# Kernel optimization log

Hardware: AMD Instinct MI355X
Metric: run time of the kernel (lower is better)

The kernel has to match this reference:

```python
import jax, jax.numpy as jnp
import numpy as np

B=16; NW=17; NR=116; WS=10; E=128; LNUM=5; NEXP=4; TOPK=2; DS=16
LAM=0.01; EPS=1e-5
ED=NW*WS      # 170 expert dim
SEQ=NR*WS     # 1160

def softshrink(x, l):
    return jnp.sign(x) * jnp.maximum(jnp.abs(x) - l, 0.0)

def layernorm(x, g, b):
    m = x.mean(-1, keepdims=True)
    v = ((x - m) ** 2).mean(-1, keepdims=True)
    return (x - m) / jnp.sqrt(v + EPS) * g + b

def sscan(x, A, WB, WC, Wdt, D):
    # Mamba-style selective scan. x: [L, d], A/WB/WC: [d, n] / [d, n_state]
    dt = jax.nn.softplus(x @ Wdt)          # [L, d]
    Bt = x @ WB                            # [L, n]
    Ct = x @ WC                            # [L, n]
    def step(h, inp):
        xt, dtt, bt, ct = inp
        dA = jnp.exp(dtt[:, None] * A)     # [d, n]
        h = dA * h + (dtt * xt)[:, None] * bt[None, :]
        y = (h * ct[None, :]).sum(-1) + D * xt
        return h, y
    h0 = jnp.zeros((x.shape[1], A.shape[1]), x.dtype)
    _, y = jax.lax.scan(step, h0, (x, dt, Bt, Ct))
    return y                               # [L, d]

def setup_inputs() -> dict:
    key = jax.random.key(0)
    ks = jax.random.split(key, 32)
    r = lambda i, sh, s=1.0: jax.random.normal(ks[i], sh, dtype=jnp.float32) * s
    return {
        'win_seq': r(0, (B, NW, NR, WS)),
        'win_pcc': r(1, (B, NR, NR, NW)),
        'global_adjs': jax.random.uniform(ks[2], (B, NR, NR), dtype=jnp.float32) / NR,
        'patch_adjs': jax.random.uniform(ks[3], (B, NW * NR, NW * NR), dtype=jnp.float32) / (NW * NR),
        'embeddings': r(4, (E,)),
        'fgc_w': r(5, (NW, LNUM, 2, E, E), 0.02),
        'fgc_b': r(6, (NW, LNUM, 2, E), 0.02),
        'w_c': r(7, (NW, E), 0.01),
        'ln_g': jnp.ones((SEQ,), jnp.float32), 'ln_b': jnp.zeros((SEQ,), jnp.float32),
        'A1': -(jax.random.uniform(ks[8], (NR, DS), dtype=jnp.float32) + 0.5),
        'WB1': r(9, (NR, DS), 0.1), 'WC1': r(10, (NR, DS), 0.1),
        'Wdt1': r(11, (NR, NR), 0.1), 'D1': jnp.ones((NR,), jnp.float32),
        'Wout1': r(12, (NW, NR, SEQ), 0.02),
        'A2': -(jax.random.uniform(ks[13], (SEQ, DS), dtype=jnp.float32) + 0.5),
        'WB2': r(14, (SEQ, DS), 0.03), 'WC2': r(15, (SEQ, DS), 0.03),
        'Wdt2': r(16, (SEQ, SEQ), 0.01), 'D2': jnp.ones((SEQ,), jnp.float32),
        'Wout2': r(17, (SEQ, SEQ), 0.02),
        'W_gate': r(18, (2 * ED, ED), 0.05), 'b_gate': jnp.zeros((ED,), jnp.float32),
        'rln_g': jnp.ones((ED,), jnp.float32), 'rln_b': jnp.zeros((ED,), jnp.float32),
        'Wr': r(19, (ED, NEXP), 0.05), 'br': jnp.zeros((NEXP,), jnp.float32),
        'We': r(20, (NEXP, ED, ED), 0.06),
        'W1': r(21, (NR * ED, 512), 0.01), 'b1': jnp.zeros((512,), jnp.float32),
        'W2': r(22, (512, 256), 0.05), 'b2': jnp.zeros((256,), jnp.float32),
        'W3': r(23, (256, 128), 0.06), 'b3': jnp.zeros((128,), jnp.float32),
        'W4': r(24, (128, 2), 0.09), 'b4': jnp.zeros((2,), jnp.float32),
    }

def reference(win_seq, win_pcc, global_adjs, patch_adjs, embeddings, fgc_w, fgc_b, w_c,
              ln_g, ln_b, A1, WB1, WC1, Wdt1, D1, Wout1, A2, WB2, WC2, Wdt2, D2, Wout2,
              W_gate, b_gate, rln_g, rln_b, Wr, br, We, W1, b1, W2, b2, W3, b3, W4, b4):
    Bsz = win_seq.shape[0]
    # tokenEmb: [B,NW,SEQ] -> [B,NW,SEQ,E]
    x = win_seq.reshape(Bsz, NW, SEQ)[..., None] * embeddings
    xf = jnp.fft.rfft(x, axis=2, norm='ortho')
    # fourierGC: 5 complex dense layers per window with relu + softshrink
    for l in range(LNUM):
        wr = fgc_w[:, l, 0]; wi = fgc_w[:, l, 1]
        br_ = fgc_b[:, l, 0]; bi_ = fgc_b[:, l, 1]
        o_r = jax.nn.relu(jnp.einsum('bwfi,wij->bwfj', xf.real, wr)
                          - jnp.einsum('bwfi,wij->bwfj', xf.imag, wi) + br_[None, :, None, :])
        o_i = jax.nn.relu(jnp.einsum('bwfi,wij->bwfj', xf.imag, wr)
                          + jnp.einsum('bwfi,wij->bwfj', xf.real, wi) + bi_[None, :, None, :])
        xf = jax.lax.complex(softshrink(o_r, LAM), softshrink(o_i, LAM))
    x = jnp.fft.irfft(xf, n=SEQ, axis=2, norm='ortho')      # [B,NW,SEQ,E]
    x = x.reshape(Bsz, NW, NR, WS, E)
    # channel-softmax pooling over embed dim (per-window w_c)
    wc = jax.nn.softmax(w_c, axis=-1)                        # [NW,E]
    freq_feat = jnp.einsum('bwnte,we->bwnt', x, wc).reshape(Bsz, NW, SEQ)

    # DGSM1: selective scan over mean-PCC node features
    x1 = win_pcc.mean(-1)                                    # [B,NR,NR]
    y1 = jax.vmap(lambda a: sscan(a, A1, WB1, WC1, Wdt1, D1))(x1)
    pooled = y1.mean(axis=1)                                 # [B,NR]
    out1 = jnp.einsum('bd,wdk->bwk', pooled, Wout1)          # [B,NW,SEQ]

    # DGSM2: graph propagation (global adjacency on roi dim) + scan over windows
    x2 = freq_feat.reshape(Bsz, NW, NR, WS)
    x2 = jnp.einsum('bnm,bwmf->bwnf', global_adjs, x2).reshape(Bsz, NW, SEQ)
    y2 = jax.vmap(lambda a: sscan(a, A2, WB2, WC2, Wdt2, D2))(x2)
    out2 = y2 @ Wout2                                        # [B,NW,SEQ]

    time_feat = layernorm(out1, ln_g, ln_b).reshape(Bsz, NW, NR, WS)
    freq2 = layernorm(out2, ln_g, ln_b).reshape(Bsz, NW, NR, WS)
    cat = jnp.concatenate([freq2, time_feat], -1).transpose(0, 2, 1, 3).reshape(Bsz, NR, 2 * ED)
    gate = jax.nn.sigmoid(cat @ W_gate + b_gate)             # [B,NR,ED]
    fp = freq2.transpose(0, 2, 1, 3).reshape(Bsz, NR, ED)
    tp = time_feat.transpose(0, 2, 1, 3).reshape(Bsz, NR, ED)
    fusion = gate * fp + (1.0 - gate) * tp                   # [B,NR,ED]

    # top-k MoE with GCN experts on global adjacency
    logits = layernorm(fusion, rln_g, rln_b) @ Wr + br       # [B,NR,NEXP]
    vals, idx = jax.lax.top_k(logits, TOPK)
    w = jax.nn.softmax(vals, axis=-1)
    gates = (jax.nn.one_hot(idx, NEXP, dtype=fusion.dtype) * w[..., None]).sum(-2)
    support = jnp.einsum('bnf,efg->beng', fusion, We)
    eout = jax.nn.relu(jnp.einsum('bnm,bemg->beng', global_adjs, support))
    moe = jnp.einsum('beng,bne->bng', eout, gates)           # [B,NR,ED]

    # classifier head; BatchNorm in eval mode with fresh running stats = x/sqrt(1+eps)
    bn_scale = 1.0 / (1.0 + EPS) ** 0.5
    h = jax.nn.relu((moe.reshape(Bsz, -1) @ W1 + b1) * bn_scale)
    h = jax.nn.relu((h @ W2 + b2) * bn_scale)
    h = jax.nn.relu((h @ W3 + b3) * bn_scale)
    return h @ W4 + b4                                       # [B,2]
```

## Files before the change

### kernel.cpp

```cpp
#include <hip/hip_runtime.h>
#include <math.h>

#define BSZ 16
#define NWW 17
#define NRR 116
#define WSS 10
#define EMB 128
#define LAYN 5
#define DST 16
#define SEQL 1160
#define FRQ 581
#define EDD 170
#define LAMW 0.01f
#define EPSW 1e-5f
#define NBW (BSZ*NWW)

#define SXF 1024.0f
#define SWF 4096.0f
#define INVS 2.384185791015625e-07f

typedef _Float16 half8 __attribute__((ext_vector_type(8)));
typedef float float4v __attribute__((ext_vector_type(4)));

__device__ __forceinline__ float softplus_f(float x){
    return fmaxf(x, 0.f) + log1pf(expf(-fabsf(x)));
}
__device__ __forceinline__ float sigmoid_f(float x){
    return 1.f / (1.f + expf(-x));
}

__global__ void k_tables(float* tc, float* ts){
    int k = blockIdx.x*256 + threadIdx.x;
    if (k < SEQL){
        double th = (6.283185307179586476925286766559 * (double)k) / (double)SEQL;
        tc[k] = (float)cos(th);
        ts[k] = (float)sin(th);
    }
}
__global__ void k_mk_tmaj(const float* tc, const float* ts, float* Ct, float* St){
    int id = blockIdx.x*256 + threadIdx.x;
    if (id >= SEQL*FRQ) return;
    int f = id % FRQ, t = id / FRQ;
    int idx = (f*t) % SEQL;
    Ct[id] = tc[idx]; St[id] = ts[idx];
}
__global__ void k_mk_fmaj(const float* tc, const float* ts, float* Cf, float* Sf){
    int id = blockIdx.x*256 + threadIdx.x;
    if (id >= SEQL*FRQ) return;
    int t = id % SEQL, f = id / SEQL;
    int idx = (f*t) % SEQL;
    Cf[id] = tc[idx]; Sf[id] = ts[idx];
}

__global__ void k_wcsm(const float* w_c, float* wcs){
    int w = blockIdx.x; int j = threadIdx.x;
    __shared__ float red[EMB];
    float v = w_c[w*EMB + j];
    red[j] = v; __syncthreads();
    for (int s = 64; s > 0; s >>= 1){ if (j < s) red[j] = fmaxf(red[j], red[j+s]); __syncthreads(); }
    float m = red[0]; __syncthreads();
    float e = expf(v - m);
    red[j] = e; __syncthreads();
    for (int s = 64; s > 0; s >>= 1){ if (j < s) red[j] += red[j+s]; __syncthreads(); }
    wcs[w*EMB + j] = e / red[0];
}

__global__ void k_ew(const float* emb, const float* fgc_w, float* ewr, float* ewi){
    int id = blockIdx.x*256 + threadIdx.x;
    if (id >= NWW*EMB) return;
    int w = id / EMB, j = id % EMB;
    const float* wr = fgc_w + ((size_t)(w*LAYN + 0)*2 + 0)*EMB*EMB;
    const float* wi = wr + (size_t)EMB*EMB;
    float ar = 0.f, ai = 0.f;
    for (int i = 0; i < EMB; i++){
        float e = emb[i];
        ar += e * wr[i*EMB + j];
        ai += e * wi[i*EMB + j];
    }
    ewr[id] = ar; ewi[id] = ai;
}

#define DFT_TCH 290
__global__ void k_dft(const float* ws, const float* Ct, const float* St,
                      float* pre, float* pim){
    __shared__ float X[4][DFT_TCH];
    int f = blockIdx.x*256 + threadIdx.x;
    int bw0 = blockIdx.y*4;
    int t0 = blockIdx.z*DFT_TCH;
    for (int e = threadIdx.x; e < 4*DFT_TCH; e += 256){
        int g = e / DFT_TCH, t = e % DFT_TCH;
        X[g][t] = ws[(size_t)(bw0+g)*SEQL + t0 + t];
    }
    __syncthreads();
    if (f >= FRQ) return;
    float sr[4] = {0,0,0,0}, si[4] = {0,0,0,0};
    #pragma unroll 2
    for (int tt = 0; tt < DFT_TCH; tt++){
        int t = t0 + tt;
        float ct_ = Ct[(size_t)t*FRQ + f];
        float st_ = St[(size_t)t*FRQ + f];
        #pragma unroll
        for (int g = 0; g < 4; g++){
            sr[g] += X[g][tt]*ct_;
            si[g] += X[g][tt]*st_;
        }
    }
    size_t base = (size_t)blockIdx.z*NBW;
    #pragma unroll
    for (int g = 0; g < 4; g++){
        pre[(base + bw0+g)*FRQ + f] = sr[g];
        pim[(base + bw0+g)*FRQ + f] = si[g];
    }
}

__global__ void k_wprep(const float* fgc_w, _Float16* Wpk){
// ... 19 lines not shown
        half8 hv, lv;
        #pragma unroll
        for (int jj = 0; jj < 8; jj++){
            int k = kc*32 + q*8 + jj;
            float v = T[k][n];
            _Float16 h = (_Float16)v;
            hv[jj] = h; lv[jj] = (_Float16)(v - (float)h);
        }
        *(half8*)&hi[d0] = hv;
        *(half8*)&lo[d0] = lv;
    }
}

#define AIDX(row, jc) (((row)<<7) + ((((jc) ^ ((row)&15))) << 3))
#define OLD 132
__launch_bounds__(256, 3)
__global__ void k_fgc_fused(const float* pre, const float* pim,
                            const float* ewr, const float* ewi,
                            const float* fgc_b, const float* wcs,
                            const _Float16* Wpk,
                            float* zre, float* zim){
    __shared__ __align__(16) _Float16 AhR[32*128];
    __shared__ __align__(16) _Float16 AlR[32*128];
    __shared__ __align__(16) _Float16 AhI[32*128];
    __shared__ __align__(16) _Float16 AlI[32*128];
    __shared__ __align__(16) float OUTR[16*OLD];
    __shared__ __align__(16) float OUTI[16*OLD];
    int tid = threadIdx.x;
    int by = blockIdx.y; int w = by >> 4; int b = by & 15;
    int bw = b*NWW + w;
    int f0 = blockIdx.x * 32;
    int lane = tid & 63, wv = tid >> 6;
    int c = lane & 15, q = lane >> 4;

    {
        int f = tid >> 3;
        int j0 = (tid & 7) << 4;
        int fg = f0 + f;
        float re = 0.f, im = 0.f;
        if (fg < FRQ){
            size_t o = (size_t)bw*FRQ + fg;
            const size_t PS = (size_t)NBW*FRQ;
            float r  = pre[o] + pre[PS+o] + pre[2*PS+o] + pre[3*PS+o];
            float i_ = pim[o] + pim[PS+o] + pim[2*PS+o] + pim[3*PS+o];
            const float sc = 0.02936128f;
            re = r * sc;
            im = -i_ * sc;
        }
        const float* br = fgc_b + (size_t)(w*LAYN + 0)*2*EMB;
        const float* bi = br + EMB;
        #pragma unroll
        for (int g = 0; g < 2; g++){
            half8 hR, lR, hI, lI;
            #pragma unroll
            for (int u = 0; u < 8; u++){
                int jj = j0 + g*8 + u;
                float er = ewr[w*EMB + jj], ei = ewi[w*EMB + jj];
                float xr = fmaxf(re*er - im*ei + br[jj] - LAMW, 0.f) * SXF;
                float xi = fmaxf(im*er + re*ei + bi[jj] - LAMW, 0.f) * SXF;
                _Float16 h1 = (_Float16)xr; hR[u] = h1; lR[u] = (_Float16)(xr - (float)h1);
                _Float16 h2 = (_Float16)xi; hI[u] = h2; lI[u] = (_Float16)(xi - (float)h2);
            }
            int jc = (tid & 7)*2 + g;
            int ao = AIDX(f, jc);
            *(half8*)&AhR[ao] = hR;
            *(half8*)&AlR[ao] = lR;
            *(half8*)&AhI[ao] = hI;
            *(half8*)&AlI[ao] = lI;
        }
    }
    __syncthreads();

    for (int l = 1; l <= 4; l++){
        const _Float16* Wb = Wpk + (size_t)(w*4 + (l-1))*65536;
        float4v Prr[2][2], Pii[2][2], Pri[2][2], Pir[2][2];
        #pragma unroll
        for (int rt = 0; rt < 2; rt++)
            #pragma unroll
            for (int ct = 0; ct < 2; ct++){
                #pragma unroll
                for (int u = 0; u < 4; u++){
                    Prr[rt][ct][u] = 0.f; Pii[rt][ct][u] = 0.f;
                    Pri[rt][ct][u] = 0.f; Pir[rt][ct][u] = 0.f;
                }
            }
        for (int kc = 0; kc < 4; kc++){
            half8 ahR[2], alR[2], ahI[2], alI[2];
            #pragma unroll
            for (int rt = 0; rt < 2; rt++){
                int ao = AIDX(rt*16 + c, kc*4 + q);
                ahR[rt] = *(const half8*)&AhR[ao];
                alR[rt] = *(const half8*)&AlR[ao];
                ahI[rt] = *(const half8*)&AhI[ao];
                alI[rt] = *(const half8*)&AlI[ao];
            }
            #pragma unroll
            for (int ct = 0; ct < 2; ct++){
                int off = ((wv*2 + ct)*2048) + kc*512 + lane*8;
                half8 whR = *(const half8*)&Wb[off];
                half8 wlR = *(const half8*)&Wb[16384 + off];
                half8 whI = *(const half8*)&Wb[32768 + off];
                half8 wlI = *(const half8*)&Wb[49152 + off];
                #pragma unroll
                for (int rt = 0; rt < 2; rt++){
                    Prr[rt][ct] = __builtin_amdgcn_mfma_f32_16x16x32_f16(ahR[rt], whR, Prr[rt][ct], 0,0,0);
                    Prr[rt][ct] = __builtin_amdgcn_mfma_f32_16x16x32_f16(ahR[rt], wlR, Prr[rt][ct], 0,0,0);
                    Prr[rt][ct] = __builtin_amdgcn_mfma_f32_16x16x32_f16(alR[rt], whR, Prr[rt][ct], 0,0,0);
                    Pii[rt][ct] = __builtin_amdgcn_mfma_f32_16x16x32_f16(ahI[rt], whI, Pii[rt][ct], 0,0,0);
                    Pii[rt][ct] = __builtin_amdgcn_mfma_f32_16x16x32_f16(ahI[rt], wlI, Pii[rt][ct], 0,0,0);
                    Pii[rt][ct] = __builtin_amdgcn_mfma_f32_16x16x32_f16(alI[rt], whI, Pii[rt][ct], 0,0,0);
                    Pri[rt][ct] = __builtin_amdgcn_mfma_f32_16x16x32_f16(ahR[rt], whI, Pri[rt][ct], 0,0,0);
                    Pri[rt][ct] = __builtin_amdgcn_mfma_f32_16x16x32_f16(ahR[rt], wlI, Pri[rt][ct], 0,0,0);
                    Pri[rt][ct] = __builtin_amdgcn_mfma_f32_16x16x32_f16(alR[rt], whI, Pri[rt][ct], 0,0,0);
                    Pir[rt][ct] = __builtin_amdgcn_mfma_f32_16x16x32_f16(ahI[rt], whR, Pir[rt][ct], 0,0,0);
                    Pir[rt][ct] = __builtin_amdgcn_mfma_f32_16x16x32_f16(ahI[rt], wlR, Pir[rt][ct], 0,0,0);
                    Pir[rt][ct] = __builtin_amdgcn_mfma_f32_16x16x32_f16(alI[rt], whR, Pir[rt][ct], 0,0,0);
                }
            }
        }
        __syncthreads();
        const float* bR = fgc_b + (size_t)(w*LAYN + l)*2*EMB;
        const float* bI = bR + EMB;
        #pragma unroll
        for (int chunk = 0; chunk < 2; chunk++){
            #pragma unroll
            for (int ct = 0; ct < 2; ct++){
                int n = wv*32 + ct*16 + c;
                float biasR = bR[n] - LAMW, biasI = bI[n] - LAMW;
                #pragma unroll
                for (int r = 0; r < 4; r++){
                    int row = q*4 + r;
                    float vR = (Prr[chunk][ct][r] - Pii[chunk][ct][r])*INVS + biasR;
                    float vI = (Pir[chunk][ct][r] + Pri[chunk][ct][r])*INVS + biasI;
                    OUTR[row*OLD + n] = fmaxf(vR, 0.f);
                    OUTI[row*OLD + n] = fmaxf(vI, 0.f);
                }
            }
            __syncthreads();
            if (l < 4){
                int fch = tid >> 4;
                int j0r = (tid & 15) << 3;
                float4v ra = *(const float4v*)&OUTR[fch*OLD + j0r];
                float4v rb = *(const float4v*)&OUTR[fch*OLD + j0r + 4];
                float4v ia = *(const float4v*)&OUTI[fch*OLD + j0r];
                float4v ib = *(const float4v*)&OUTI[fch*OLD + j0r + 4];
                half8 hR, lR, hI, lI;
                #pragma unroll
                for (int u = 0; u < 4; u++){
                    float xr = ra[u] * SXF;
                    float xi = ia[u] * SXF;
                    _Float16 h1 = (_Float16)xr; hR[u] = h1; lR[u] = (_Float16)(xr - (float)h1);
                    _Float16 h2 = (_Float16)xi; hI[u] = h2; lI[u] = (_Float16)(xi - (float)h2);
                }
                #pragma unroll
                for (int u = 0; u < 4; u++){
                    float xr = rb[u] * SXF;
                    float xi = ib[u] * SXF;
                    _Float16 h1 = (_Float16)xr; hR[4+u] = h1; lR[4+u] = (_Float16)(xr - (float)h1);
                    _Float16 h2 = (_Float16)xi; hI[4+u] = h2; lI[4+u] = (_Float16)(xi - (float)h2);
                }
                int ao = AIDX(chunk*16 + fch, (tid & 15));
                *(half8*)&AhR[ao] = hR;
                *(half8*)&AlR[ao] = lR;
                *(half8*)&AhI[ao] = hI;
                *(half8*)&AlI[ao] = lI;
            } else {
                int fch = tid >> 4;
                int j0r = (tid & 15) << 3;
                float4v ra = *(const float4v*)&OUTR[fch*OLD + j0r];
                float4v rb = *(const float4v*)&OUTR[fch*OLD + j0r + 4];
                float4v ia = *(const float4v*)&OUTI[fch*OLD + j0r];
                float4v ib = *(const float4v*)&OUTI[fch*OLD + j0r + 4];
                float sR = 0.f, sI = 0.f;
                #pragma unroll
                for (int u = 0; u < 4; u++){
                    float cwa = wcs[w*EMB + j0r + u];
                    float cwb = wcs[w*EMB + j0r + 4 + u];
                    sR += ra[u]*cwa + rb[u]*cwb;
                    sI += ia[u]*cwa + ib[u]*cwb;
                }
                #pragma unroll
                for (int o = 8; o > 0; o >>= 1){
                    sR += __shfl_down(sR, o, 64);
                    sI += __shfl_down(sI, o, 64);
                }
                int fg = f0 + chunk*16 + fch;
                if ((tid & 15) == 0 && fg < FRQ){
                    zre[(size_t)bw*FRQ + fg] = sR;
                    zim[(size_t)bw*FRQ + fg] = sI;
                }
            }
            __syncthreads();
        }
    }
}

#define IR_FCH 145
__global__ void k_irfft(const float* zre, const float* zim, const float* Cf, const float* Sf,
                        float* part){
    __shared__ float ZR[4][IR_FCH+1];
    __shared__ float ZI[4][IR_FCH+1];
    int t = blockIdx.x*256 + threadIdx.x;
    int bw0 = blockIdx.y*4;
    int f0 = 1 + blockIdx.z*IR_FCH;
    int fn = min(f0 + IR_FCH, FRQ-1) - f0;
    for (int e = threadIdx.x; e < 4*fn; e += 256){
        int g = e / fn, f = e % fn;
        ZR[g][f] = zre[(size_t)(bw0+g)*FRQ + f0 + f];
        ZI[g][f] = zim[(size_t)(bw0+g)*FRQ + f0 + f];
    }
    __syncthreads();
    if (t >= SEQL) return;
    float acc[4] = {0,0,0,0};
    #pragma unroll 2
    for (int ff_ = 0; ff_ < fn; ff_++){
        int f = f0 + ff_;
        float cf = Cf[(size_t)f*SEQL + t];
        float sf = Sf[(size_t)f*SEQL + t];
        #pragma unroll
        for (int g = 0; g < 4; g++)
            acc[g] += ZR[g][ff_]*cf - ZI[g][ff_]*sf;
    }
    size_t base = (size_t)blockIdx.z*NBW;
    #pragma unroll
    for (int g = 0; g < 4; g++)
        part[(base + bw0+g)*SEQL + t] = acc[g];
}
__global__ void k_irfftc(const float* part, const float* zre, float* ff){
    int id = blockIdx.x*256 + threadIdx.x;
    if (id >= NBW*SEQL) return;
    int t = id % SEQL; int bw = id / SEQL;
    const size_t NS = (size_t)NBW*SEQL;
    float s = part[id] + part[NS + id] + part[2*NS + id] + part[3*NS + id];
// ... 39 lines not shown
    float a = A1[c*DST + s];
    float h = 0.f, csum = 0.f, xsum = 0.f;
    for (int t = 0; t < NRR; t++){
        size_t o = (size_t)(b*NRR + t)*NRR + c;
        float dtv = dt1[o], xv = x1[o];
        size_t ro = (size_t)(b*NRR + t)*DST + s;
        h = expf(dtv*a)*h + dtv*xv*BT1[ro];
        csum += h*CT1[ro];
        xsum += xv;
    }
    #pragma unroll
    for (int o = 8; o > 0; o >>= 1) csum += __shfl_xor(csum, o, 16);
    if (s == 0) pooled[bc] = (csum + D1[c]*xsum) * (1.f/NRR);
}
__global__ void k_out1(const float* pooled, const float* Wout1, float* out1){
    int id = blockIdx.x*256 + threadIdx.x;
    if (id >= NBW*SEQL) return;
    int k = id % SEQL; int bw = id / SEQL; int w = bw % NWW; int b = bw / NWW;
    float s = 0.f;
    for (int d = 0; d < NRR; d++) s += pooled[b*NRR + d] * Wout1[((size_t)w*NRR + d)*SEQL + k];
    out1[id] = s;
}

__global__ void k_ln(const float* in, const float* g, const float* bta, float* out){
    __shared__ float row[SEQL];
    __shared__ float red[256];
    int r = blockIdx.x; int tid = threadIdx.x;
    const float* x = in + (size_t)r*SEQL;
    float s = 0.f;
    for (int i = tid; i < SEQL; i += 256){ float v = x[i]; row[i] = v; s += v; }
    red[tid] = s; __syncthreads();
    for (int st = 128; st > 0; st >>= 1){ if (tid < st) red[tid] += red[tid+st]; __syncthreads(); }
    float m = red[0] * (1.f/SEQL); __syncthreads();
    float vs = 0.f;
    for (int i = tid; i < SEQL; i += 256){ float d = row[i] - m; vs += d*d; }
    red[tid] = vs; __syncthreads();
// ... 26 lines not shown
}

__global__ void k_x2(const float* ga, const float* ff, float* x2){
    int id = blockIdx.x*256 + threadIdx.x;
    if (id >= NBW*SEQL) return;
    int within = id % SEQL; int q = within % WSS; int n = within / WSS;
    int bw = id / SEQL; int w = bw % NWW; int b = bw / NWW;
    const float* gr = ga + ((size_t)b*NRR + n)*NRR;
    const float* fr = ff + (size_t)(b*NWW + w)*SEQL + q;
    float s = 0.f;
    for (int m = 0; m < NRR; m++) s += gr[m] * fr[m*WSS];
    x2[id] = s;
}
#define DT_MCH 290
__global__ void k_dt2(const float* x2, const float* Wdt2, float* part){
    __shared__ float X[4][DT_MCH];
    int c = blockIdx.x*256 + threadIdx.x;
    int bt0 = blockIdx.y*4;
    int m0 = blockIdx.z*DT_MCH;
    for (int e = threadIdx.x; e < 4*DT_MCH; e += 256){
        int g = e / DT_MCH, m = e % DT_MCH;
        X[g][m] = x2[(size_t)(bt0+g)*SEQL + m0 + m];
    }
    __syncthreads();
    if (c >= SEQL) return;
    float a[4] = {0,0,0,0};
    #pragma unroll 2
    for (int mm = 0; mm < DT_MCH; mm++){
        float wv_ = Wdt2[(size_t)(m0+mm)*SEQL + c];
        #pragma unroll
        for (int g = 0; g < 4; g++) a[g] += X[g][mm]*wv_;
    }
    size_t base = (size_t)blockIdx.z*NBW;
    #pragma unroll
    for (int g = 0; g < 4; g++)
        part[(base + bt0+g)*SEQL + c] = a[g];
}
__global__ void k_btct2(const float* x2, const float* WB2, const float* WC2,
                        float* BT2, float* CT2){
    __shared__ float SB[256], SC[256];
    int bt = blockIdx.x;
    int tid = threadIdx.x;
    int s = tid & 15, mc = tid >> 4;
    int m0 = mc*73, m1 = min(m0 + 73, SEQL);
    const float* xr = x2 + (size_t)bt*SEQL;
    float sb = 0.f, sc = 0.f;
    for (int m = m0; m < m1; m++){
        float v = xr[m];
        sb += v*WB2[m*DST + s];
        sc += v*WC2[m*DST + s];
// ... 23 lines not shown
        float dtv = softplus_f(dtp[o] + dtp[NS+o] + dtp[2*NS+o] + dtp[3*NS+o]);
        float xv = x2[o];
        float dx = dtv * xv;
        const float* bt = BT2 + (size_t)(b*NWW + t)*DST;
        const float* ct = CT2 + (size_t)(b*NWW + t)*DST;
        float y = dv * xv;
        #pragma unroll
        for (int s = 0; s < DST; s++){
            h[s] = expf(dtv*a[s])*h[s] + dx*bt[s];
            y += h[s]*ct[s];
        }
        y2[o] = y;
    }
}
__global__ void k_out2(const float* y2, const float* Wout2, float* part){
    __shared__ float Y[4][DT_MCH];
    int k = blockIdx.x*256 + threadIdx.x;
    int bw0 = blockIdx.y*4;
    int m0 = blockIdx.z*DT_MCH;
    for (int e = threadIdx.x; e < 4*DT_MCH; e += 256){
        int g = e / DT_MCH, m = e % DT_MCH;
        Y[g][m] = y2[(size_t)(bw0+g)*SEQL + m0 + m];
    }
    __syncthreads();
    if (k >= SEQL) return;
    float a[4] = {0,0,0,0};
    #pragma unroll 2
    for (int mm = 0; mm < DT_MCH; mm++){
        float wv_ = Wout2[(size_t)(m0+mm)*SEQL + k];
        #pragma unroll
        for (int g = 0; g < 4; g++) a[g] += Y[g][mm]*wv_;
    }
    size_t base = (size_t)blockIdx.z*NBW;
    #pragma unroll
    for (int g = 0; g < 4; g++)
        part[(base + bw0+g)*SEQL + k] = a[g];
}

__global__ void k_gatefusion(const float* fr2, const float* tf, const float* W_gate,
                             const float* b_gate, float* fusion){
    int id = blockIdx.x*256 + threadIdx.x;
    if (id >= BSZ*NRR*EDD) return;
    int j = id % EDD; int n = (id / EDD) % NRR; int b = id / (EDD*NRR);
    float acc = b_gate[j];
    for (int w = 0; w < NWW; w++){
        const float* f2 = fr2 + (size_t)(b*NWW + w)*SEQL + n*WSS;
        const float* tp = tf  + (size_t)(b*NWW + w)*SEQL + n*WSS;
        const float* wg = W_gate + (size_t)(w*2*WSS)*EDD + j;
        #pragma unroll
        for (int q = 0; q < WSS; q++) acc += f2[q]*wg[q*EDD];
// ... 71 lines not shown
    eout[id] = fmaxf(s, 0.f);
}
__global__ void k_moe(const float* eout, const float* gatesE, float* moe){
    int id = blockIdx.x*256 + threadIdx.x;
    if (id >= BSZ*NRR*EDD) return;
    int g = id % EDD; int n = (id / EDD) % NRR; int b = id / (EDD*NRR);
    const float* gt = gatesE + ((size_t)b*NRR + n)*4;
    float s = 0.f;
    #pragma unroll
    for (int e = 0; e < 4; e++)
        s += eout[((size_t)(b*4 + e)*NRR + n)*EDD + g] * gt[e];
    moe[id] = s;
}

#define MLPK (NRR*EDD)
#define KSPLIT 80
#define KCH 247
__global__ void k_mlp1p(const float* moe, const float* W1, float* part1){
    __shared__ float M[16*KCH];
    int kc = blockIdx.x;
    int j = blockIdx.y*256 + threadIdx.x;
    int i0 = kc*KCH; int len = MLPK - i0; if (len > KCH) len = KCH;
    for (int e = threadIdx.x; e < 16*len; e += 256){
        int b = e / len, i = e % len;
        M[b*KCH + i] = moe[(size_t)b*MLPK + i0 + i];
    }
    __syncthreads();
    float acc[16];
    #pragma unroll
    for (int b = 0; b < 16; b++) acc[b] = 0.f;
    for (int i = 0; i < len; i++){
        float wv_ = W1[(size_t)(i0+i)*512 + j];
// ... 76 lines not shown
    const float* We      = (const float*)d_in[28];
    const float* W1      = (const float*)d_in[29];
    const float* b1      = (const float*)d_in[30];
    const float* W2      = (const float*)d_in[31];
    const float* b2      = (const float*)d_in[32];
    const float* W3      = (const float*)d_in[33];
    const float* b3      = (const float*)d_in[34];
    const float* W4      = (const float*)d_in[35];
    const float* b4      = (const float*)d_in[36];
    float* out = (float*)d_out;
    float* ws  = (float*)d_ws;

    size_t off = 0;
    auto alloc = [&](size_t n){ size_t o = off; off += (n + 63) & ~(size_t)63; return o; };
    size_t o_tabc = alloc(SEQL), o_tabs = alloc(SEQL);
    size_t o_Ct = alloc((size_t)SEQL*FRQ), o_St = alloc((size_t)SEQL*FRQ);
    size_t o_Cf = alloc((size_t)SEQL*FRQ), o_Sf = alloc((size_t)SEQL*FRQ);
    size_t o_wcs = alloc(NWW*EMB);
    size_t o_ewr = alloc(NWW*EMB), o_ewi = alloc(NWW*EMB);
    size_t o_wpk = alloc((size_t)2228224);
    size_t o_zre = alloc((size_t)NBW*FRQ), o_zim = alloc((size_t)NBW*FRQ);
    size_t o_ff  = alloc((size_t)NBW*SEQL);
    size_t o_pa  = alloc((size_t)4*NBW*SEQL);
    size_t o_pb  = alloc((size_t)4*NBW*FRQ);
    size_t o_x1  = alloc((size_t)BSZ*NRR*NRR);
    size_t o_dt1 = alloc((size_t)BSZ*NRR*NRR);
    size_t o_BT1 = alloc((size_t)BSZ*NRR*DST), o_CT1 = alloc((size_t)BSZ*NRR*DST);
    size_t o_pool= alloc((size_t)BSZ*NRR);
    size_t o_o1  = alloc((size_t)NBW*SEQL);
    size_t o_tf  = alloc((size_t)NBW*SEQL);
    size_t o_x2  = alloc((size_t)NBW*SEQL);
    size_t o_BT2 = alloc((size_t)NBW*DST), o_CT2 = alloc((size_t)NBW*DST);
    size_t o_y2  = alloc((size_t)NBW*SEQL);
    size_t o_fr2 = alloc((size_t)NBW*SEQL);
    size_t o_fus = alloc((size_t)BSZ*NRR*EDD);
    size_t o_gte = alloc((size_t)BSZ*NRR*4);
    size_t o_sup = alloc((size_t)BSZ*4*NRR*EDD);
    size_t o_eo  = alloc((size_t)BSZ*4*NRR*EDD);
    size_t o_moe = alloc((size_t)BSZ*NRR*EDD);
    size_t o_p1  = alloc((size_t)KSPLIT*BSZ*512);
    size_t o_h1  = alloc((size_t)BSZ*512);
    size_t o_h2  = alloc((size_t)BSZ*256);
    size_t o_h3  = alloc((size_t)BSZ*128);
    if (ws_size < off*sizeof(float)) return;

    #define WSP(o) (ws + (o))
    int nMk = (SEQL*FRQ + 255)/256;
    k_tables<<<(SEQL+255)/256, 256, 0, stream>>>(WSP(o_tabc), WSP(o_tabs));
    k_mk_tmaj<<<nMk, 256, 0, stream>>>(WSP(o_tabc), WSP(o_tabs), WSP(o_Ct), WSP(o_St));
    k_mk_fmaj<<<nMk, 256, 0, stream>>>(WSP(o_tabc), WSP(o_tabs), WSP(o_Cf), WSP(o_Sf));
    k_wcsm<<<NWW, EMB, 0, stream>>>(w_c, WSP(o_wcs));
    k_ew<<<(NWW*EMB+255)/256, 256, 0, stream>>>(emb, fgc_w, WSP(o_ewr), WSP(o_ewi));
    k_wprep<<<136, 256, 0, stream>>>(fgc_w, (_Float16*)WSP(o_wpk));
    k_dft<<<dim3(3, 68, 4), 256, 0, stream>>>(win_seq, WSP(o_Ct), WSP(o_St), WSP(o_pa), WSP(o_pb));
    k_fgc_fused<<<dim3(19, NBW), 256, 0, stream>>>(WSP(o_pa), WSP(o_pb), WSP(o_ewr), WSP(o_ewi),
                                                   fgc_b, WSP(o_wcs),
                                                   (const _Float16*)WSP(o_wpk),
                                                   WSP(o_zre), WSP(o_zim));
    k_irfft<<<dim3(5, 68, 4), 256, 0, stream>>>(WSP(o_zre), WSP(o_zim), WSP(o_Cf), WSP(o_Sf), WSP(o_pa));
    k_irfftc<<<(NBW*SEQL+255)/256, 256, 0, stream>>>(WSP(o_pa), WSP(o_zre), WSP(o_ff));
    k_x1mean<<<(BSZ*NRR*NRR+255)/256, 256, 0, stream>>>(win_pcc, WSP(o_x1));
    k_dt1<<<(BSZ*NRR*NRR+255)/256, 256, 0, stream>>>(WSP(o_x1), Wdt1, WSP(o_dt1));
    k_btct1<<<(BSZ*NRR*DST+255)/256, 256, 0, stream>>>(WSP(o_x1), WB1, WC1, WSP(o_BT1), WSP(o_CT1));
    k_sscan1<<<(BSZ*NRR*DST+255)/256, 256, 0, stream>>>(WSP(o_x1), WSP(o_dt1), WSP(o_BT1), WSP(o_CT1),
                                                        A1, D1, WSP(o_pool));
    k_out1<<<(NBW*SEQL+255)/256, 256, 0, stream>>>(WSP(o_pool), Wout1, WSP(o_o1));
    k_ln<<<NBW, 256, 0, stream>>>(WSP(o_o1), ln_g, ln_b, WSP(o_tf));
    k_x2<<<(NBW*SEQL+255)/256, 256, 0, stream>>>(ga, WSP(o_ff), WSP(o_x2));
    k_dt2<<<dim3(5, 68, 4), 256, 0, stream>>>(WSP(o_x2), Wdt2, WSP(o_pa));
    k_btct2<<<NBW, 256, 0, stream>>>(WSP(o_x2), WB2, WC2, WSP(o_BT2), WSP(o_CT2));
    k_sscan2<<<(BSZ*SEQL+255)/256, 256, 0, stream>>>(WSP(o_x2), WSP(o_pa), WSP(o_BT2), WSP(o_CT2),
                                                     A2, D2, WSP(o_y2));
    k_out2<<<dim3(5, 68, 4), 256, 0, stream>>>(WSP(o_y2), Wout2, WSP(o_pa));
    k_ln4<<<NBW, 256, 0, stream>>>(WSP(o_pa), ln_g, ln_b, WSP(o_fr2));
    k_gatefusion<<<(BSZ*NRR*EDD+255)/256, 256, 0, stream>>>(WSP(o_fr2), WSP(o_tf), W_gate, b_gate, WSP(o_fus));
    k_gates<<<BSZ*NRR, 64, 0, stream>>>(WSP(o_fus), rln_g, rln_b, Wr, brr, WSP(o_gte));
    k_support<<<(BSZ*4*NRR*EDD+255)/256, 256, 0, stream>>>(WSP(o_fus), We, WSP(o_sup));
    k_eout<<<(BSZ*4*NRR*EDD+255)/256, 256, 0, stream>>>(ga, WSP(o_sup), WSP(o_eo));
    k_moe<<<(BSZ*NRR*EDD+255)/256, 256, 0, stream>>>(WSP(o_eo), WSP(o_gte), WSP(o_moe));
    k_mlp1p<<<dim3(KSPLIT, 2), 256, 0, stream>>>(WSP(o_moe), W1, WSP(o_p1));
    k_mlp1c<<<(BSZ*512)/256, 256, 0, stream>>>(WSP(o_p1), b1, WSP(o_h1));
    k_mlp2<<<(BSZ*256)/256, 256, 0, stream>>>(WSP(o_h1), W2, b2, WSP(o_h2));
    k_mlp3<<<(BSZ*128+255)/256, 256, 0, stream>>>(WSP(o_h2), W3, b3, WSP(o_h3));
    k_mlp4<<<1, 64, 0, stream>>>(WSP(o_h3), W4, b4, out);
    #undef WSP
}
```

Baseline: 1.296 ms.

## Replace DFT twiddle matrices with LDS tables, retile FGC and GEMV kernels

Removes the two large precomputed cos/sin matrices and their build kernels. The DFT and inverse-DFT kernels now read a 1160-entry twiddle table staged in LDS, stepping the index modularly. k_fgc_fused moves to 512 threads with one column tile per wave, halving per-thread accumulators. k_out1 reuses each weight load across 4 batches, k_dt2/k_out2 reuse each weight load across 16 rows, and the MLP K-split is doubled. This cuts global-memory traffic and table build time, at the cost of more LDS use, more registers in the dt2/out2 kernels, and fewer blocks launched there.

Measured after the change: 1.310 ms. Within noise of the previous version (+1.1%).

```diff
diff --git a/kernel.cpp b/kernel.cpp
--- a/kernel.cpp
+++ b/kernel.cpp
@@ -37,20 +37,6 @@
         ts[k] = (float)sin(th);
     }
 }
-__global__ void k_mk_tmaj(const float* tc, const float* ts, float* Ct, float* St){
-    int id = blockIdx.x*256 + threadIdx.x;
-    if (id >= SEQL*FRQ) return;
-    int f = id % FRQ, t = id / FRQ;
-    int idx = (f*t) % SEQL;
-    Ct[id] = tc[idx]; St[id] = ts[idx];
-}
-__global__ void k_mk_fmaj(const float* tc, const float* ts, float* Cf, float* Sf){
-    int id = blockIdx.x*256 + threadIdx.x;
-    if (id >= SEQL*FRQ) return;
-    int t = id % SEQL, f = id / SEQL;
-    int idx = (f*t) % SEQL;
-    Cf[id] = tc[idx]; Sf[id] = ts[idx];
-}
 
 __global__ void k_wcsm(const float* w_c, float* wcs){
     int w = blockIdx.x; int j = threadIdx.x;
@@ -81,9 +67,11 @@
 }
 
 #define DFT_TCH 290
-__global__ void k_dft(const float* ws, const float* Ct, const float* St,
+__global__ void k_dft(const float* ws, const float* tabc, const float* tabs,
                       float* pre, float* pim){
     __shared__ float X[4][DFT_TCH];
+    __shared__ float TTC[SEQL];
+    __shared__ float TTS[SEQL];
     int f = blockIdx.x*256 + threadIdx.x;
     int bw0 = blockIdx.y*4;
     int t0 = blockIdx.z*DFT_TCH;
@@ -91,14 +79,18 @@
         int g = e / DFT_TCH, t = e % DFT_TCH;
         X[g][t] = ws[(size_t)(bw0+g)*SEQL + t0 + t];
     }
+    for (int i = threadIdx.x; i < SEQL; i += 256){
+        TTC[i] = tabc[i]; TTS[i] = tabs[i];
+    }
     __syncthreads();
     if (f >= FRQ) return;
     float sr[4] = {0,0,0,0}, si[4] = {0,0,0,0};
+    int idx = (f * t0) % SEQL;
     #pragma unroll 2
     for (int tt = 0; tt < DFT_TCH; tt++){
-        int t = t0 + tt;
-        float ct_ = Ct[(size_t)t*FRQ + f];
-        float st_ = St[(size_t)t*FRQ + f];
+        float ct_ = TTC[idx];
+        float st_ = TTS[idx];
+        idx += f; if (idx >= SEQL) idx -= SEQL;
         #pragma unroll
         for (int g = 0; g < 4; g++){
             sr[g] += X[g][tt]*ct_;
@@ -148,7 +140,7 @@
 
 #define AIDX(row, jc) (((row)<<7) + ((((jc) ^ ((row)&15))) << 3))
 #define OLD 132
-__launch_bounds__(256, 3)
+__launch_bounds__(512, 6)
 __global__ void k_fgc_fused(const float* pre, const float* pim,
                             const float* ewr, const float* ewi,
                             const float* fgc_b, const float* wcs,
@@ -168,8 +160,8 @@
     int c = lane & 15, q = lane >> 4;
 
     {
-        int f = tid >> 3;
-        int j0 = (tid & 7) << 4;
+        int f = tid >> 4;
+        int j0 = (tid & 15) << 3;
         int fg = f0 + f;
         float re = 0.f, im = 0.f;
         if (fg < FRQ){
@@ -183,41 +175,35 @@
         }
         const float* br = fgc_b + (size_t)(w*LAYN + 0)*2*EMB;
         const float* bi = br + EMB;
-        #pragma unroll
-        for (int g = 0; g < 2; g++){
-            half8 hR, lR, hI, lI;
-            #pragma unroll
-            for (int u = 0; u < 8; u++){
-                int jj = j0 + g*8 + u;
-                float er = ewr[w*EMB + jj], ei = ewi[w*EMB + jj];
-                float xr = fmaxf(re*er - im*ei + br[jj] - LAMW, 0.f) * SXF;
-                float xi = fmaxf(im*er + re*ei + bi[jj] - LAMW, 0.f) * SXF;
-                _Float16 h1 = (_Float16)xr; hR[u] = h1; lR[u] = (_Float16)(xr - (float)h1);
-                _Float16 h2 = (_Float16)xi; hI[u] = h2; lI[u] = (_Float16)(xi - (float)h2);
-            }
-            int jc = (tid & 7)*2 + g;
-            int ao = AIDX(f, jc);
-            *(half8*)&AhR[ao] = hR;
-            *(half8*)&AlR[ao] = lR;
-            *(half8*)&AhI[ao] = hI;
-            *(half8*)&AlI[ao] = lI;
+        half8 hR, lR, hI, lI;
+        #pragma unroll
+        for (int u = 0; u < 8; u++){
+            int jj = j0 + u;
+            float er = ewr[w*EMB + jj], ei = ewi[w*EMB + jj];
+            float xr = fmaxf(re*er - im*ei + br[jj] - LAMW, 0.f) * SXF;
+            float xi = fmaxf(im*er + re*ei + bi[jj] - LAMW, 0.f) * SXF;
+            _Float16 h1 = (_Float16)xr; hR[u] = h1; lR[u] = (_Float16)(xr - (float)h1);
+            _Float16 h2 = (_Float16)xi; hI[u] = h2; lI[u] = (_Float16)(xi - (float)h2);
         }
+        int ao = AIDX(f, (tid & 15));
+        *(half8*)&AhR[ao] = hR;
+        *(half8*)&AlR[ao] = lR;
+        *(half8*)&AhI[ao] = hI;
+        *(half8*)&AlI[ao] = lI;
     }
     __syncthreads();
 
     for (int l = 1; l <= 4; l++){
         const _Float16* Wb = Wpk + (size_t)(w*4 + (l-1))*65536;
-        float4v Prr[2][2], Pii[2][2], Pri[2][2], Pir[2][2];
-        #pragma unroll
-        for (int rt = 0; rt < 2; rt++)
+        float4v Prr[2], Pii[2], Pri[2], Pir[2];
+        #pragma unroll
+        for (int rt = 0; rt < 2; rt++){
             #pragma unroll
-            for (int ct = 0; ct < 2; ct++){
-                #pragma unroll
-                for (int u = 0; u < 4; u++){
-                    Prr[rt][ct][u] = 0.f; Pii[rt][ct][u] = 0.f;
-                    Pri[rt][ct][u] = 0.f; Pir[rt][ct][u] = 0.f;
-                }
+            for (int u = 0; u < 4; u++){
+                Prr[rt][u] = 0.f; Pii[rt][u] = 0.f;
+                Pri[rt][u] = 0.f; Pir[rt][u] = 0.f;
             }
+        }
         for (int kc = 0; kc < 4; kc++){
             half8 ahR[2], alR[2], ahI[2], alI[2];
             #pragma unroll
@@ -228,28 +214,25 @@
                 ahI[rt] = *(const half8*)&AhI[ao];
                 alI[rt] = *(const half8*)&AlI[ao];
             }
+            int off = wv*2048 + kc*512 + lane*8;
+            half8 whR = *(const half8*)&Wb[off];
+            half8 wlR = *(const half8*)&Wb[16384 + off];
+            half8 whI = *(const half8*)&Wb[32768 + off];
+            half8 wlI = *(const half8*)&Wb[49152 + off];
             #pragma unroll
-            for (int ct = 0; ct < 2; ct++){
-                int off = ((wv*2 + ct)*2048) + kc*512 + lane*8;
-                half8 whR = *(const half8*)&Wb[off];
-                half8 wlR = *(const half8*)&Wb[16384 + off];
-                half8 whI = *(const half8*)&Wb[32768 + off];
-                half8 wlI = *(const half8*)&Wb[49152 + off];
-                #pragma unroll
-                for (int rt = 0; rt < 2; rt++){
-                    Prr[rt][ct] = __builtin_amdgcn_mfma_f32_16x16x32_f16(ahR[rt], whR, Prr[rt][ct], 0,0,0);
-                    Prr[rt][ct] = __builtin_amdgcn_mfma_f32_16x16x32_f16(ahR[rt], wlR, Prr[rt][ct], 0,0,0);
-                    Prr[rt][ct] = __builtin_amdgcn_mfma_f32_16x16x32_f16(alR[rt], whR, Prr[rt][ct], 0,0,0);
-                    Pii[rt][ct] = __builtin_amdgcn_mfma_f32_16x16x32_f16(ahI[rt], whI, Pii[rt][ct], 0,0,0);
-                    Pii[rt][ct] = __builtin_amdgcn_mfma_f32_16x16x32_f16(ahI[rt], wlI, Pii[rt][ct], 0,0,0);
-                    Pii[rt][ct] = __builtin_amdgcn_mfma_f32_16x16x32_f16(alI[rt], whI, Pii[rt][ct], 0,0,0);
-                    Pri[rt][ct] = __builtin_amdgcn_mfma_f32_16x16x32_f16(ahR[rt], whI, Pri[rt][ct], 0,0,0);
-                    Pri[rt][ct] = __builtin_amdgcn_mfma_f32_16x16x32_f16(ahR[rt], wlI, Pri[rt][ct], 0,0,0);
-                    Pri[rt][ct] = __builtin_amdgcn_mfma_f32_16x16x32_f16(alR[rt], whI, Pri[rt][ct], 0,0,0);
-                    Pir[rt][ct] = __builtin_amdgcn_mfma_f32_16x16x32_f16(ahI[rt], whR, Pir[rt][ct], 0,0,0);
-                    Pir[rt][ct] = __builtin_amdgcn_mfma_f32_16x16x32_f16(ahI[rt], wlR, Pir[rt][ct], 0,0,0);
-                    Pir[rt][ct] = __builtin_amdgcn_mfma_f32_16x16x32_f16(alI[rt], whR, Pir[rt][ct], 0,0,0);
-                }
+            for (int rt = 0; rt < 2; rt++){
+                Prr[rt] = __builtin_amdgcn_mfma_f32_16x16x32_f16(ahR[rt], whR, Prr[rt], 0,0,0);
+                Prr[rt] = __builtin_amdgcn_mfma_f32_16x16x32_f16(ahR[rt], wlR, Prr[rt], 0,0,0);
+                Prr[rt] = __builtin_amdgcn_mfma_f32_16x16x32_f16(alR[rt], whR, Prr[rt], 0,0,0);
+                Pii[rt] = __builtin_amdgcn_mfma_f32_16x16x32_f16(ahI[rt], whI, Pii[rt], 0,0,0);
+                Pii[rt] = __builtin_amdgcn_mfma_f32_16x16x32_f16(ahI[rt], wlI, Pii[rt], 0,0,0);
+                Pii[rt] = __builtin_amdgcn_mfma_f32_16x16x32_f16(alI[rt], whI, Pii[rt], 0,0,0);
+                Pri[rt] = __builtin_amdgcn_mfma_f32_16x16x32_f16(ahR[rt], whI, Pri[rt], 0,0,0);
+                Pri[rt] = __builtin_amdgcn_mfma_f32_16x16x32_f16(ahR[rt], wlI, Pri[rt], 0,0,0);
+                Pri[rt] = __builtin_amdgcn_mfma_f32_16x16x32_f16(alR[rt], whI, Pri[rt], 0,0,0);
+                Pir[rt] = __builtin_amdgcn_mfma_f32_16x16x32_f16(ahI[rt], whR, Pir[rt], 0,0,0);
+                Pir[rt] = __builtin_amdgcn_mfma_f32_16x16x32_f16(ahI[rt], wlR, Pir[rt], 0,0,0);
+                Pir[rt] = __builtin_amdgcn_mfma_f32_16x16x32_f16(alI[rt], whR, Pir[rt], 0,0,0);
             }
         }
         __syncthreads();
@@ -257,71 +240,74 @@
         const float* bI = bR + EMB;
         #pragma unroll
         for (int chunk = 0; chunk < 2; chunk++){
-            #pragma unroll
-            for (int ct = 0; ct < 2; ct++){
-                int n = wv*32 + ct*16 + c;
+            {
+                int n = wv*16 + c;
                 float biasR = bR[n] - LAMW, biasI = bI[n] - LAMW;
                 #pragma unroll
                 for (int r = 0; r < 4; r++){
                     int row = q*4 + r;
-                    float vR = (Prr[chunk][ct][r] - Pii[chunk][ct][r])*INVS + biasR;
-                    float vI = (Pir[chunk][ct][r] + Pri[chunk][ct][r])*INVS + biasI;
+                    float vR = (Prr[chunk][r] - Pii[chunk][r])*INVS + biasR;
+                    float vI = (Pir[chunk][r] + Pri[chunk][r])*INVS + biasI;
                     OUTR[row*OLD + n] = fmaxf(vR, 0.f);
                     OUTI[row*OLD + n] = fmaxf(vI, 0.f);
                 }
             }
             __syncthreads();
             if (l < 4){
-                int fch = tid >> 4;
-                int j0r = (tid & 15) << 3;
-                float4v ra = *(const float4v*)&OUTR[fch*OLD + j0r];
-                float4v rb = *(const float4v*)&OUTR[fch*OLD + j0r + 4];
-                float4v ia = *(const float4v*)&OUTI[fch*OLD + j0r];
-                float4v ib = *(const float4v*)&OUTI[fch*OLD + j0r + 4];
-                half8 hR, lR, hI, lI;
-                #pragma unroll
-                for (int u = 0; u < 4; u++){
-                    float xr = ra[u] * SXF;
-                    float xi = ia[u] * SXF;
-                    _Float16 h1 = (_Float16)xr; hR[u] = h1; lR[u] = (_Float16)(xr - (float)h1);
-                    _Float16 h2 = (_Float16)xi; hI[u] = h2; lI[u] = (_Float16)(xi - (float)h2);
+                if (tid < 256){
+                    int fch = tid >> 4;
+                    int j0r = (tid & 15) << 3;
+                    float4v ra = *(const float4v*)&OUTR[fch*OLD + j0r];
+                    float4v rb = *(const float4v*)&OUTR[fch*OLD + j0r + 4];
+                    float4v ia = *(const float4v*)&OUTI[fch*OLD + j0r];
+                    float4v ib = *(const float4v*)&OUTI[fch*OLD + j0r + 4];
+                    half8 hR, lR, hI, lI;
+                    #pragma unroll
+                    for (int u = 0; u < 4; u++){
+                        float xr = ra[u] * SXF;
+                        float xi = ia[u] * SXF;
+                        _Float16 h1 = (_Float16)xr; hR[u] = h1; lR[u] = (_Float16)(xr - (float)h1);
+                        _Float16 h2 = (_Float16)xi; hI[u] = h2; lI[u] = (_Float16)(xi - (float)h2);
+                    }
+                    #pragma unroll
+                    for (int u = 0; u < 4; u++){
+                        float xr = rb[u] * SXF;
+                        float xi = ib[u] * SXF;
+                        _Float16 h1 = (_Float16)xr; hR[4+u] = h1; lR[4+u] = (_Float16)(xr - (float)h1);
+                        _Float16 h2 = (_Float16)xi; hI[4+u] = h2; lI[4+u] = (_Float16)(xi - (float)h2);
+                    }
+                    int ao = AIDX(chunk*16 + fch, (tid & 15));
+                    *(half8*)&AhR[ao] = hR;
+                    *(half8*)&AlR[ao] = lR;
+                    *(half8*)&AhI[ao] = hI;
+                    *(half8*)&AlI[ao] = lI;
                 }
-                #pragma unroll
-                for (int u = 0; u < 4; u++){
-                    float xr = rb[u] * SXF;
-                    float xi = ib[u] * SXF;
-                    _Float16 h1 = (_Float16)xr; hR[4+u] = h1; lR[4+u] = (_Float16)(xr - (float)h1);
-                    _Float16 h2 = (_Float16)xi; hI[4+u] = h2; lI[4+u] = (_Float16)(xi - (float)h2);
-                }
-                int ao = AIDX(chunk*16 + fch, (tid & 15));
-                *(half8*)&AhR[ao] = hR;
-                *(half8*)&AlR[ao] = lR;
-                *(half8*)&AhI[ao] = hI;
-                *(half8*)&AlI[ao] = lI;
             } else {
-                int fch = tid >> 4;
-                int j0r = (tid & 15) << 3;
-                float4v ra = *(const float4v*)&OUTR[fch*OLD + j0r];
-                float4v rb = *(const float4v*)&OUTR[fch*OLD + j0r + 4];
-                float4v ia = *(const float4v*)&OUTI[fch*OLD + j0r];
-                float4v ib = *(const float4v*)&OUTI[fch*OLD + j0r + 4];
-                float sR = 0.f, sI = 0.f;
-                #pragma unroll
-                for (int u = 0; u < 4; u++){
-                    float cwa = wcs[w*EMB + j0r + u];
-                    float cwb = wcs[w*EMB + j0r + 4 + u];
-                    sR += ra[u]*cwa + rb[u]*cwb;
-                    sI += ia[u]*cwa + ib[u]*cwb;
-                }
-                #pragma unroll
-                for (int o = 8; o > 0; o >>= 1){
-                    sR += __shfl_down(sR, o, 64);
-                    sI += __shfl_down(sI, o, 64);
-                }
-                int fg = f0 + chunk*16 + fch;
-                if ((tid & 15) == 0 && fg < FRQ){
-                    zre[(size_t)bw*FRQ + fg] = sR;
-                    zim[(size_t)bw*FRQ + fg] = sI;
+                if (tid < 256){
+                    int fch = tid >> 4;
+                    int j0r = (tid & 15) << 3;
+                    float4v ra = *(const float4v*)&OUTR[fch*OLD + j0r];
+                    float4v rb = *(const float4v*)&OUTR[fch*OLD + j0r + 4];
+                    float4v ia = *(const float4v*)&OUTI[fch*OLD + j0r];
+                    float4v ib = *(const float4v*)&OUTI[fch*OLD + j0r + 4];
+                    float sR = 0.f, sI = 0.f;
+                    #pragma unroll
+                    for (int u = 0; u < 4; u++){
+                        float cwa = wcs[w*EMB + j0r + u];
+                        float cwb = wcs[w*EMB + j0r + 4 + u];
+                        sR += ra[u]*cwa + rb[u]*cwb;
+                        sI += ia[u]*cwa + ib[u]*cwb;
+                    }
+                    #pragma unroll
+                    for (int o = 8; o > 0; o >>= 1){
+                        sR += __shfl_down(sR, o, 64);
+                        sI += __shfl_down(sI, o, 64);
+                    }
+                    int fg = f0 + chunk*16 + fch;
+                    if ((tid & 15) == 0 && fg < FRQ){
+                        zre[(size_t)bw*FRQ + fg] = sR;
+                        zim[(size_t)bw*FRQ + fg] = sI;
+                    }
                 }
             }
             __syncthreads();
@@ -330,10 +316,12 @@
 }
 
 #define IR_FCH 145
-__global__ void k_irfft(const float* zre, const float* zim, const float* Cf, const float* Sf,
+__global__ void k_irfft(const float* zre, const float* zim, const float* tabc, const float* tabs,
                         float* part){
     __shared__ float ZR[4][IR_FCH+1];
     __shared__ float ZI[4][IR_FCH+1];
+    __shared__ float TTC[SEQL];
+    __shared__ float TTS[SEQL];
     int t = blockIdx.x*256 + threadIdx.x;
     int bw0 = blockIdx.y*4;
     int f0 = 1 + blockIdx.z*IR_FCH;
@@ -343,14 +331,18 @@
         ZR[g][f] = zre[(size_t)(bw0+g)*FRQ + f0 + f];
         ZI[g][f] = zim[(size_t)(bw0+g)*FRQ + f0 + f];
     }
+    for (int i = threadIdx.x; i < SEQL; i += 256){
+        TTC[i] = tabc[i]; TTS[i] = tabs[i];
+    }
     __syncthreads();
     if (t >= SEQL) return;
     float acc[4] = {0,0,0,0};
+    int idx = (t * f0) % SEQL;
     #pragma unroll 2
     for (int ff_ = 0; ff_ < fn; ff_++){
-        int f = f0 + ff_;
-        float cf = Cf[(size_t)f*SEQL + t];
-        float sf = Sf[(size_t)f*SEQL + t];
+        float cf = TTC[idx];
+        float sf = TTS[idx];
+        idx += t; if (idx >= SEQL) idx -= SEQL;
         #pragma unroll
         for (int g = 0; g < 4; g++)
             acc[g] += ZR[g][ff_]*cf - ZI[g][ff_]*sf;
@@ -420,12 +412,23 @@
     if (s == 0) pooled[bc] = (csum + D1[c]*xsum) * (1.f/NRR);
 }
 __global__ void k_out1(const float* pooled, const float* Wout1, float* out1){
-    int id = blockIdx.x*256 + threadIdx.x;
-    if (id >= NBW*SEQL) return;
-    int k = id % SEQL; int bw = id / SEQL; int w = bw % NWW; int b = bw / NWW;
-    float s = 0.f;
-    for (int d = 0; d < NRR; d++) s += pooled[b*NRR + d] * Wout1[((size_t)w*NRR + d)*SEQL + k];
-    out1[id] = s;
+    int k = blockIdx.x*256 + threadIdx.x;
+    int w = blockIdx.y;
+    int b0 = blockIdx.z*4;
+    if (k >= SEQL) return;
+    const float* Wp = Wout1 + (size_t)w*NRR*SEQL + k;
+    float a0 = 0.f, a1 = 0.f, a2 = 0.f, a3 = 0.f;
+    for (int d = 0; d < NRR; d++){
+        float wv_ = Wp[(size_t)d*SEQL];
+        a0 += pooled[(b0+0)*NRR + d]*wv_;
+        a1 += pooled[(b0+1)*NRR + d]*wv_;
+        a2 += pooled[(b0+2)*NRR + d]*wv_;
+        a3 += pooled[(b0+3)*NRR + d]*wv_;
+    }
+    out1[((size_t)(b0+0)*NWW + w)*SEQL + k] = a0;
+    out1[((size_t)(b0+1)*NWW + w)*SEQL + k] = a1;
+    out1[((size_t)(b0+2)*NWW + w)*SEQL + k] = a2;
+    out1[((size_t)(b0+3)*NWW + w)*SEQL + k] = a3;
 }
 
 __global__ void k_ln(const float* in, const float* g, const float* bta, float* out){
@@ -482,26 +485,27 @@
 }
 #define DT_MCH 290
 __global__ void k_dt2(const float* x2, const float* Wdt2, float* part){
-    __shared__ float X[4][DT_MCH];
+    __shared__ float X[16][DT_MCH];
     int c = blockIdx.x*256 + threadIdx.x;
-    int bt0 = blockIdx.y*4;
+    int bt0 = blockIdx.y*16;
     int m0 = blockIdx.z*DT_MCH;
-    for (int e = threadIdx.x; e < 4*DT_MCH; e += 256){
+    for (int e = threadIdx.x; e < 16*DT_MCH; e += 256){
         int g = e / DT_MCH, m = e % DT_MCH;
         X[g][m] = x2[(size_t)(bt0+g)*SEQL + m0 + m];
     }
     __syncthreads();
     if (c >= SEQL) return;
-    float a[4] = {0,0,0,0};
-    #pragma unroll 2
+    float a[16];
+    #pragma unroll
+    for (int g = 0; g < 16; g++) a[g] = 0.f;
     for (int mm = 0; mm < DT_MCH; mm++){
         float wv_ = Wdt2[(size_t)(m0+mm)*SEQL + c];
         #pragma unroll
-        for (int g = 0; g < 4; g++) a[g] += X[g][mm]*wv_;
+        for (int g = 0; g < 16; g++) a[g] += X[g][mm]*wv_;
     }
     size_t base = (size_t)blockIdx.z*NBW;
     #pragma unroll
-    for (int g = 0; g < 4; g++)
+    for (int g = 0; g < 16; g++)
         part[(base + bt0+g)*SEQL + c] = a[g];
 }
 __global__ void k_btct2(const float* x2, const float* WB2, const float* WC2,
@@ -555,26 +559,27 @@
     }
 }
 __global__ void k_out2(const float* y2, const float* Wout2, float* part){
-    __shared__ float Y[4][DT_MCH];
+    __shared__ float Y[16][DT_MCH];
     int k = blockIdx.x*256 + threadIdx.x;
-    int bw0 = blockIdx.y*4;
+    int bw0 = blockIdx.y*16;
     int m0 = blockIdx.z*DT_MCH;
-    for (int e = threadIdx.x; e < 4*DT_MCH; e += 256){
+    for (int e = threadIdx.x; e < 16*DT_MCH; e += 256){
         int g = e / DT_MCH, m = e % DT_MCH;
         Y[g][m] = y2[(size_t)(bw0+g)*SEQL + m0 + m];
     }
     __syncthreads();
     if (k >= SEQL) return;
-    float a[4] = {0,0,0,0};
-    #pragma unroll 2
+    float a[16];
+    #pragma unroll
+    for (int g = 0; g < 16; g++) a[g] = 0.f;
     for (int mm = 0; mm < DT_MCH; mm++){
         float wv_ = Wout2[(size_t)(m0+mm)*SEQL + k];
         #pragma unroll
-        for (int g = 0; g < 4; g++) a[g] += Y[g][mm]*wv_;
+        for (int g = 0; g < 16; g++) a[g] += Y[g][mm]*wv_;
     }
     size_t base = (size_t)blockIdx.z*NBW;
     #pragma unroll
-    for (int g = 0; g < 4; g++)
+    for (int g = 0; g < 16; g++)
         part[(base + bw0+g)*SEQL + k] = a[g];
 }
 
@@ -676,8 +681,8 @@
 }
 
 #define MLPK (NRR*EDD)
-#define KSPLIT 80
-#define KCH 247
+#define KSPLIT 160
+#define KCH 124
 __global__ void k_mlp1p(const float* moe, const float* W1, float* part1){
     __shared__ float M[16*KCH];
     int kc = blockIdx.x;
@@ -784,8 +789,6 @@
     size_t off = 0;
     auto alloc = [&](size_t n){ size_t o = off; off += (n + 63) & ~(size_t)63; return o; };
     size_t o_tabc = alloc(SEQL), o_tabs = alloc(SEQL);
-    size_t o_Ct = alloc((size_t)SEQL*FRQ), o_St = alloc((size_t)SEQL*FRQ);
-    size_t o_Cf = alloc((size_t)SEQL*FRQ), o_Sf = alloc((size_t)SEQL*FRQ);
     size_t o_wcs = alloc(NWW*EMB);
     size_t o_ewr = alloc(NWW*EMB), o_ewi = alloc(NWW*EMB);
     size_t o_wpk = alloc((size_t)2228224);
@@ -815,33 +818,30 @@
     if (ws_size < off*sizeof(float)) return;
 
     #define WSP(o) (ws + (o))
-    int nMk = (SEQL*FRQ + 255)/256;
     k_tables<<<(SEQL+255)/256, 256, 0, stream>>>(WSP(o_tabc), WSP(o_tabs));
-    k_mk_tmaj<<<nMk, 256, 0, stream>>>(WSP(o_tabc), WSP(o_tabs), WSP(o_Ct), WSP(o_St));
-    k_mk_fmaj<<<nMk, 256, 0, stream>>>(WSP(o_tabc), WSP(o_tabs), WSP(o_Cf), WSP(o_Sf));
     k_wcsm<<<NWW, EMB, 0, stream>>>(w_c, WSP(o_wcs));
     k_ew<<<(NWW*EMB+255)/256, 256, 0, stream>>>(emb, fgc_w, WSP(o_ewr), WSP(o_ewi));
     k_wprep<<<136, 256, 0, stream>>>(fgc_w, (_Float16*)WSP(o_wpk));
-    k_dft<<<dim3(3, 68, 4), 256, 0, stream>>>(win_seq, WSP(o_Ct), WSP(o_St), WSP(o_pa), WSP(o_pb));
-    k_fgc_fused<<<dim3(19, NBW), 256, 0, stream>>>(WSP(o_pa), WSP(o_pb), WSP(o_ewr), WSP(o_ewi),
+    k_dft<<<dim3(3, 68, 4), 256, 0, stream>>>(win_seq, WSP(o_tabc), WSP(o_tabs), WSP(o_pa), WSP(o_pb));
+    k_fgc_fused<<<dim3(19, NBW), 512, 0, stream>>>(WSP(o_pa), WSP(o_pb), WSP(o_ewr), WSP(o_ewi),
                                                    fgc_b, WSP(o_wcs),
                                                    (const _Float16*)WSP(o_wpk),
                                                    WSP(o_zre), WSP(o_zim));
-    k_irfft<<<dim3(5, 68, 4), 256, 0, stream>>>(WSP(o_zre), WSP(o_zim), WSP(o_Cf), WSP(o_Sf), WSP(o_pa));
+    k_irfft<<<dim3(5, 68, 4), 256, 0, stream>>>(WSP(o_zre), WSP(o_zim), WSP(o_tabc), WSP(o_tabs), WSP(o_pa));
     k_irfftc<<<(NBW*SEQL+255)/256, 256, 0, stream>>>(WSP(o_pa), WSP(o_zre), WSP(o_ff));
     k_x1mean<<<(BSZ*NRR*NRR+255)/256, 256, 0, stream>>>(win_pcc, WSP(o_x1));
     k_dt1<<<(BSZ*NRR*NRR+255)/256, 256, 0, stream>>>(WSP(o_x1), Wdt1, WSP(o_dt1));
     k_btct1<<<(BSZ*NRR*DST+255)/256, 256, 0, stream>>>(WSP(o_x1), WB1, WC1, WSP(o_BT1), WSP(o_CT1));
     k_sscan1<<<(BSZ*NRR*DST+255)/256, 256, 0, stream>>>(WSP(o_x1), WSP(o_dt1), WSP(o_BT1), WSP(o_CT1),
                                                         A1, D1, WSP(o_pool));
-    k_out1<<<(NBW*SEQL+255)/256, 256, 0, stream>>>(WSP(o_pool), Wout1, WSP(o_o1));
+    k_out1<<<dim3(5, 17, 4), 256, 0, stream>>>(WSP(o_pool), Wout1, WSP(o_o1));
     k_ln<<<NBW, 256, 0, stream>>>(WSP(o_o1), ln_g, ln_b, WSP(o_tf));
     k_x2<<<(NBW*SEQL+255)/256, 256, 0, stream>>>(ga, WSP(o_ff), WSP(o_x2));
-    k_dt2<<<dim3(5, 68, 4), 256, 0, stream>>>(WSP(o_x2), Wdt2, WSP(o_pa));
+    k_dt2<<<dim3(5, 17, 4), 256, 0, stream>>>(WSP(o_x2), Wdt2, WSP(o_pa));
     k_btct2<<<NBW, 256, 0, stream>>>(WSP(o_x2), WB2, WC2, WSP(o_BT2), WSP(o_CT2));
     k_sscan2<<<(BSZ*SEQL+255)/256, 256, 0, stream>>>(WSP(o_x2), WSP(o_pa), WSP(o_BT2), WSP(o_CT2),
                                                      A2, D2, WSP(o_y2));
-    k_out2<<<dim3(5, 68, 4), 256, 0, stream>>>(WSP(o_y2), Wout2, WSP(o_pa));
+    k_out2<<<dim3(5, 17, 4), 256, 0, stream>>>(WSP(o_y2), Wout2, WSP(o_pa));
     k_ln4<<<NBW, 256, 0, stream>>>(WSP(o_pa), ln_g, ln_b, WSP(o_fr2));
     k_gatefusion<<<(BSZ*NRR*EDD+255)/256, 256, 0, stream>>>(WSP(o_fr2), WSP(o_tf), W_gate, b_gate, WSP(o_fus));
     k_gates<<<BSZ*NRR, 64, 0, stream>>>(WSP(o_fus), rln_g, rln_b, Wr, brr, WSP(o_gte));
```
